# Performance work log

Hardware: AMD Instinct MI355X
Metric: run time of the kernel (lower is better)

The kernel has to match this reference:

```python
import jax, jax.numpy as jnp
import numpy as np

COMMITMENT = 1.0

def setup_inputs() -> dict:
    key = jax.random.key(0)
    k1, k2 = jax.random.split(key)
    x = jax.random.normal(k1, (32, 64, 64, 64), dtype=jnp.float32)       # [B, D, H, W]
    emb_w = jax.random.normal(k2, (512, 64), dtype=jnp.float32)          # [K, D] codebook
    return {"x": x, "emb_w": emb_w}

def reference(x, emb_w):
    B, D, H, W = x.shape
    K = emb_w.shape[0]
    # permute channels last and flatten: [B*H*W, D]
    xp = jnp.transpose(x, (0, 2, 3, 1))
    flat = xp.reshape(-1, D)
    # squared-distance matrix [N, K] via ||a||^2 + ||b||^2 - 2 a.b
    distances = (jnp.sum(flat * flat, axis=1, keepdims=True)
                 + jnp.sum(emb_w * emb_w, axis=1)
                 - 2.0 * jnp.matmul(flat, emb_w.T))
    encoding_flat = jnp.argmin(distances, axis=1)                        # [N]
    quantized = emb_w[encoding_flat].reshape(B, H, W, D)                 # gather
    quantized = jnp.transpose(quantized, (0, 3, 1, 2))                   # back to [B, D, H, W]
    # commitment loss: mse(stop_grad(quantized), x)
    e_latent_loss = jnp.mean((jax.lax.stop_gradient(quantized) - x) ** 2)
    loss = COMMITMENT * e_latent_loss
    # straight-through estimator
    quantized_st = x + jax.lax.stop_gradient(quantized - x)
    encoding = encoding_flat.reshape(B, H, W)
    return quantized_st, encoding, distances, loss
```

## Files before the change

kernel.cpp:

```cpp
#include <hip/hip_runtime.h>

typedef short short8 __attribute__((ext_vector_type(8)));
typedef float f32x4 __attribute__((ext_vector_type(4)));

#define EPS 0.012f

__device__ __forceinline__ unsigned short rne_bf16(float v) {
    unsigned u = __float_as_uint(v);
    unsigned r = u + 0x7FFFu + ((u >> 16) & 1u);
    return (unsigned short)(r >> 16);
}
__device__ __forceinline__ float bf16_to_f(unsigned short h) {
    return __uint_as_float(((unsigned)h) << 16);
}
__device__ __forceinline__ int xsw(int row, int d4) {
    return row * 64 + (d4 ^ ((row & 15) << 2));
}

#define MFMA(a,b,c) __builtin_amdgcn_mfma_f32_16x16x32_bf16((a),(b),(c),0,0,0)

__global__ __launch_bounds__(512, 4) void vq_kernel(
    const float* __restrict__ x, const float* __restrict__ emb,
    float* __restrict__ out_q, float* __restrict__ out_enc,
    float* __restrict__ out_dist, float* __restrict__ out_loss)
{
    __shared__ __align__(16) float xs[128 * 64];
    __shared__ __align__(16) unsigned short ehi[128 * 64];
    __shared__ __align__(16) unsigned short elo[128 * 64];
    __shared__ float xpart[4][128];
    __shared__ float xx_s[128];
    __shared__ float ee_s[128];
    __shared__ int   enc_s[128];
    __shared__ float red_s[8];

    const int t   = threadIdx.x;
    const int bid = blockIdx.x;
    const int n_base = bid * 128;
    const int b   = bid >> 5;
    const int h0  = (bid & 31) * 2;
    const size_t xb0 = (size_t)b * 262144 + (size_t)h0 * 64;
    const int l  = t & 63;
    const int wv = t >> 6;

    {
        const int w  = t & 63;
        const int q  = t >> 6;
        const int hh = q & 1;
        const int c0 = q >> 1;
        const int row = hh * 64 + w;
        const size_t gb = xb0 + hh * 64 + w;
        float part = 0.f;
        #pragma unroll
        for (int cc = 0; cc < 4; ++cc) {
            int d4 = (c0 + cc * 4) * 4;
            float4 v;
            v.x = x[gb + (size_t)(d4 + 0) * 4096];
            v.y = x[gb + (size_t)(d4 + 1) * 4096];
            v.z = x[gb + (size_t)(d4 + 2) * 4096];
            v.w = x[gb + (size_t)(d4 + 3) * 4096];
            part = fmaf(v.x, v.x, part); part = fmaf(v.y, v.y, part);
            part = fmaf(v.z, v.z, part); part = fmaf(v.w, v.w, part);
            *(float4*)&xs[xsw(row, d4)] = v;
        }
        xpart[c0][row] = part;
    }
    __syncthreads();
    if (t < 128) xx_s[t] = (xpart[0][t] + xpart[1][t]) + (xpart[2][t] + xpart[3][t]);

    const int arow = wv * 16 + (l & 15);
    const int ad0  = (l >> 4) * 8;
    short8 ahi0, ahi1, alo0, alo1;
    {
        float va[16];
        *(float4*)&va[0]  = *(const float4*)&xs[xsw(arow, ad0)];
        *(float4*)&va[4]  = *(const float4*)&xs[xsw(arow, ad0 + 4)];
        *(float4*)&va[8]  = *(const float4*)&xs[xsw(arow, ad0 + 32)];
        *(float4*)&va[12] = *(const float4*)&xs[xsw(arow, ad0 + 36)];
        #pragma unroll
        for (int i = 0; i < 8; ++i) {
            unsigned short hb = rne_bf16(va[i]);
            ahi0[i] = (short)hb; alo0[i] = (short)rne_bf16(va[i] - bf16_to_f(hb));
            unsigned short hb2 = rne_bf16(va[8 + i]);
            ahi1[i] = (short)hb2; alo1[i] = (short)rne_bf16(va[8 + i] - bf16_to_f(hb2));
        }
    }
    __syncthreads();

    const int rlw0 = (l >> 4) * 4;
    const int n0   = n_base + wv * 16 + rlw0;
    float xx4[4];
    #pragma unroll
    for (int r = 0; r < 4; ++r) xx4[r] = xx_s[wv * 16 + rlw0 + r];

    float m1[4], m2[4]; int k1[4];
    #pragma unroll
    for (int r = 0; r < 4; ++r) { m1[r] = 3.4e38f; m2[r] = 3.4e38f; k1[r] = 0; }

    float* dbase = out_dist + (size_t)n0 * 512 + (l & 15);

    for (int kc = 0; kc < 4; ++kc) {
        __syncthreads();
        float s01[2];
        #pragma unroll
        for (int it = 0; it < 2; ++it) {
            int flat = t + it * 512;
            int kr = flat >> 3;
            int d0 = (flat & 7) * 8;
            const float* src = emb + (size_t)(kc * 128 + kr) * 64 + d0;
            float4 v0 = *(const float4*)src;
            float4 v1 = *(const float4*)(src + 4);
            float vv[8] = {v0.x, v0.y, v0.z, v0.w, v1.x, v1.y, v1.z, v1.w};
            short8 h8, l8; float s = 0.f;
            #pragma unroll
            for (int i = 0; i < 8; ++i) {
                s = fmaf(vv[i], vv[i], s);
                unsigned short hb = rne_bf16(vv[i]);
                h8[i] = (short)hb; l8[i] = (short)rne_bf16(vv[i] - bf16_to_f(hb));
            }
            int idx = kr * 64 + (d0 ^ ((kr & 7) << 3));
            *(short8*)&ehi[idx] = h8;
            *(short8*)&elo[idx] = l8;
            s01[it] = s;
        }
        #pragma unroll
        for (int m = 1; m < 8; m <<= 1) {
            s01[0] += __shfl_xor(s01[0], m, 64);
            s01[1] += __shfl_xor(s01[1], m, 64);
        }
        if ((t & 7) == 0) {
            ee_s[t >> 3]        = s01[0];
            ee_s[64 + (t >> 3)] = s01[1];
        }
        __syncthreads();

        #pragma unroll 1
        for (int kt = 0; kt < 8; ++kt) {
            int kl  = kt * 16 + (l & 15);
            int bix = kl * 64;
            int bsw = (kl & 7) << 3;
            int bd0 = (l >> 4) * 8;
            short8 bh0 = *(short8*)&ehi[bix + (bd0 ^ bsw)];
            short8 bh1 = *(short8*)&ehi[bix + ((bd0 + 32) ^ bsw)];
            short8 bl0 = *(short8*)&elo[bix + (bd0 ^ bsw)];
            short8 bl1 = *(short8*)&elo[bix + ((bd0 + 32) ^ bsw)];
            f32x4 accA = {0.f, 0.f, 0.f, 0.f};
            f32x4 accB = {0.f, 0.f, 0.f, 0.f};
            accA = MFMA(ahi0, bh0, accA);
            accB = MFMA(ahi1, bh1, accB);
            accA = MFMA(alo0, bh0, accA);
            accB = MFMA(alo1, bh1, accB);
            accA = MFMA(ahi0, bl0, accA);
            accB = MFMA(ahi1, bl1, accB);
            float eek = ee_s[kl];
            int kg = kc * 128 + kl;
            float* dp = dbase + kc * 128 + kt * 16;
            #pragma unroll
            for (int r = 0; r < 4; ++r) {
                float dist = fmaf(accA[r] + accB[r], -2.f, xx4[r] + eek);
                dp[(size_t)r * 512] = dist;
                if (dist < m1[r]) { m2[r] = m1[r]; m1[r] = dist; k1[r] = kg; }
                else if (dist < m2[r]) m2[r] = dist;
            }
        }
    }

    __syncthreads();

    float lacc = 0.f;
    {
        const unsigned long long gmask = 0xFFFFull << ((l >> 4) << 4);
        #pragma unroll 1
        for (int r = 0; r < 4; ++r) {
            float bv = m1[r]; int bk = k1[r];
            #pragma unroll
            for (int m = 1; m < 16; m <<= 1) {
                float ov = __shfl_xor(bv, m, 64);
                int   ok = __shfl_xor(bk, m, 64);
                if (ov < bv || (ov == bv && ok < bk)) { bv = ov; bk = ok; }
            }
            float thr = bv + EPS;
            unsigned long long b1 = __ballot(m1[r] <= thr);
            unsigned long long b2 = __ballot(m2[r] <= thr);
            int enc = bk; float lossv = bv;
            if (__popcll(b1 & gmask) > 1 || (b2 & gmask) != 0ULL) {
                const int rowg = wv * 16 + rlw0 + r;
                const float* drow = out_dist + (size_t)(n_base + rowg) * 512 + (l & 15) * 32;
                double bestv = 1e300; int bestk = 0x7fffffff;
                #pragma unroll 1
                for (int c4 = 0; c4 < 8; ++c4) {
                    float4 dv = *(const float4*)(drow + c4 * 4);
                    float dvv[4] = {dv.x, dv.y, dv.z, dv.w};
                    #pragma unroll 1
                    for (int j = 0; j < 4; ++j) {
                        if (dvv[j] <= thr) {
                            int k = (l & 15) * 32 + c4 * 4 + j;
                            const float* er = emb + k * 64;
                            double s = 0.0;
                            #pragma unroll 4
                            for (int d = 0; d < 64; d += 4) {
                                float4 ev = *(const float4*)(er + d);
                                float4 xv = *(const float4*)&xs[xsw(rowg, d)];
                                double d0_ = (double)xv.x - (double)ev.x;
                                double d1_ = (double)xv.y - (double)ev.y;
                                double d2_ = (double)xv.z - (double)ev.z;
                                double d3_ = (double)xv.w - (double)ev.w;
                                s += d0_ * d0_ + d1_ * d1_ + d2_ * d2_ + d3_ * d3_;
                            }
                            if (s < bestv) { bestv = s; bestk = k; }
                        }
                    }
                }
                #pragma unroll
                for (int m = 1; m < 16; m <<= 1) {
                    double ov = __shfl_xor(bestv, m, 64);
                    int   ok  = __shfl_xor(bestk, m, 64);
                    if (ov < bestv || (ov == bestv && ok < bestk)) { bestv = ov; bestk = ok; }
                }
                enc = bestk;
                if ((l & 15) == 0 && enc != bk)
                    lossv = out_dist[(size_t)(n_base + rowg) * 512 + enc];
            }
            if ((l & 15) == 0) {
                enc_s[wv * 16 + rlw0 + r] = enc;
                out_enc[n0 + r] = (float)enc;
                lacc += lossv;
            }
        }
    }
    #pragma unroll
    for (int m = 32; m >= 1; m >>= 1) lacc += __shfl_down(lacc, m, 64);
    if (l == 0) red_s[wv] = lacc;
    __syncthreads();
    if (t == 0) {
        float tot = 0.f;
        #pragma unroll
        for (int i = 0; i < 8; ++i) tot += red_s[i];
        atomicAdd(out_loss, tot * (1.0f / 8388608.0f));
    }

    {
        const int w   = t & 63;
        const int q   = t >> 6;
        const int hh  = q & 1;
        const int dg  = q >> 1;
        const int row = hh * 64 + w;
        const int e   = enc_s[row];
        const float* er = emb + e * 64 + dg * 16;
        float* qp = out_q + xb0 + (size_t)(dg * 16) * 4096 + hh * 64 + w;
        #pragma unroll
        for (int qi = 0; qi < 4; ++qi) {
            float4 q4 = *(const float4*)(er + qi * 4);
            qp[(size_t)(qi * 4 + 0) * 4096] = q4.x;
            qp[(size_t)(qi * 4 + 1) * 4096] = q4.y;
            qp[(size_t)(qi * 4 + 2) * 4096] = q4.z;
            qp[(size_t)(qi * 4 + 3) * 4096] = q4.w;
        }
    }
}

extern "C" void kernel_launch(void* const* d_in, const int* in_sizes, int n_in,
                              void* d_out, int out_size, void* d_ws, size_t ws_size,
                              hipStream_t stream) {
    const float* x   = (const float*)d_in[0];
    const float* emb = (const float*)d_in[1];

    float* out_q    = (float*)d_out;
    float* out_enc  = out_q + 8388608;
    float* out_dist = out_enc + 131072;
    float* out_loss = out_dist + 67108864;

    hipMemsetAsync(out_loss, 0, sizeof(float), stream);
    vq_kernel<<<1024, 512, 0, stream>>>(x, emb, out_q, out_enc, out_dist, out_loss);
}
```

Measured before the change: 111.6 us.

## Precompute bf16 hi/lo codebook in prep kernel and stream B operands from global

Adds a small prep kernel that splits the codebook into bf16 hi/lo halves, pre-arranged in MFMA fragment order, and computes the row norms into workspace. The main kernel no longer converts the codebook per block into LDS. It reads B fragments straight from global/L2 with no per-chunk barriers. Blocks shrink to 64 rows and 256 threads with a 2048-block grid, cutting LDS use and raising occupancy. The cost is an extra kernel launch, and every block now fetches the codebook from global memory instead of shared memory.

```diff
diff --git a/kernel.cpp b/kernel.cpp
--- a/kernel.cpp
+++ b/kernel.cpp
@@ -19,36 +19,57 @@
 
 #define MFMA(a,b,c) __builtin_amdgcn_mfma_f32_16x16x32_bf16((a),(b),(c),0,0,0)
 
-__global__ __launch_bounds__(512, 4) void vq_kernel(
+__global__ __launch_bounds__(64) void prep_kernel(
+    const float* __restrict__ emb, unsigned short* __restrict__ whi,
+    unsigned short* __restrict__ wlo, float* __restrict__ wee)
+{
+    const int k = blockIdx.x * 64 + threadIdx.x;
+    const float* src = emb + k * 64;
+    float nrm = 0.f;
+    #pragma unroll
+    for (int g = 0; g < 8; ++g) {
+        float4 v0 = *(const float4*)(src + g * 8);
+        float4 v1 = *(const float4*)(src + g * 8 + 4);
+        float vv[8] = {v0.x, v0.y, v0.z, v0.w, v1.x, v1.y, v1.z, v1.w};
+        short8 h8, l8;
+        #pragma unroll
+        for (int i = 0; i < 8; ++i) {
+            nrm = fmaf(vv[i], vv[i], nrm);
+            unsigned short hb = rne_bf16(vv[i]);
+            h8[i] = (short)hb;
+            l8[i] = (short)rne_bf16(vv[i] - bf16_to_f(hb));
+        }
+        *(short8*)(whi + k * 64 + g * 8) = h8;
+        *(short8*)(wlo + k * 64 + g * 8) = l8;
+    }
+    wee[k] = nrm;
+}
+
+__global__ __launch_bounds__(256, 5) void vq_kernel(
     const float* __restrict__ x, const float* __restrict__ emb,
+    const unsigned short* __restrict__ whi, const unsigned short* __restrict__ wlo,
+    const float* __restrict__ wee,
     float* __restrict__ out_q, float* __restrict__ out_enc,
     float* __restrict__ out_dist, float* __restrict__ out_loss)
 {
-    __shared__ __align__(16) float xs[128 * 64];
-    __shared__ __align__(16) unsigned short ehi[128 * 64];
-    __shared__ __align__(16) unsigned short elo[128 * 64];
-    __shared__ float xpart[4][128];
-    __shared__ float xx_s[128];
-    __shared__ float ee_s[128];
-    __shared__ int   enc_s[128];
-    __shared__ float red_s[8];
+    __shared__ __align__(16) float xs[64 * 64];
+    __shared__ float ee_s[512];
+    __shared__ float xpart[4][64];
+    __shared__ float xx_s[64];
+    __shared__ int   enc_s[64];
+    __shared__ float red_s[4];
 
     const int t   = threadIdx.x;
     const int bid = blockIdx.x;
-    const int n_base = bid * 128;
-    const int b   = bid >> 5;
-    const int h0  = (bid & 31) * 2;
-    const size_t xb0 = (size_t)b * 262144 + (size_t)h0 * 64;
+    const int n_base = bid * 64;
+    const size_t xbase = (size_t)(bid >> 6) * 262144 + (size_t)(bid & 63) * 64;
     const int l  = t & 63;
     const int wv = t >> 6;
 
     {
         const int w  = t & 63;
-        const int q  = t >> 6;
-        const int hh = q & 1;
-        const int c0 = q >> 1;
-        const int row = hh * 64 + w;
-        const size_t gb = xb0 + hh * 64 + w;
+        const int c0 = t >> 6;
+        const size_t gb = xbase + w;
         float part = 0.f;
         #pragma unroll
         for (int cc = 0; cc < 4; ++cc) {
@@ -60,12 +81,14 @@
             v.w = x[gb + (size_t)(d4 + 3) * 4096];
             part = fmaf(v.x, v.x, part); part = fmaf(v.y, v.y, part);
             part = fmaf(v.z, v.z, part); part = fmaf(v.w, v.w, part);
-            *(float4*)&xs[xsw(row, d4)] = v;
-        }
-        xpart[c0][row] = part;
-    }
-    __syncthreads();
-    if (t < 128) xx_s[t] = (xpart[0][t] + xpart[1][t]) + (xpart[2][t] + xpart[3][t]);
+            *(float4*)&xs[xsw(w, d4)] = v;
+        }
+        xpart[c0][w] = part;
+        ee_s[t]       = wee[t];
+        ee_s[t + 256] = wee[t + 256];
+    }
+    __syncthreads();
+    if (t < 64) xx_s[t] = (xpart[0][t] + xpart[1][t]) + (xpart[2][t] + xpart[3][t]);
 
     const int arow = wv * 16 + (l & 15);
     const int ad0  = (l >> 4) * 8;
@@ -97,70 +120,34 @@
     for (int r = 0; r < 4; ++r) { m1[r] = 3.4e38f; m2[r] = 3.4e38f; k1[r] = 0; }
 
     float* dbase = out_dist + (size_t)n0 * 512 + (l & 15);
-
-    for (int kc = 0; kc < 4; ++kc) {
-        __syncthreads();
-        float s01[2];
-        #pragma unroll
-        for (int it = 0; it < 2; ++it) {
-            int flat = t + it * 512;
-            int kr = flat >> 3;
-            int d0 = (flat & 7) * 8;
-            const float* src = emb + (size_t)(kc * 128 + kr) * 64 + d0;
-            float4 v0 = *(const float4*)src;
-            float4 v1 = *(const float4*)(src + 4);
-            float vv[8] = {v0.x, v0.y, v0.z, v0.w, v1.x, v1.y, v1.z, v1.w};
-            short8 h8, l8; float s = 0.f;
-            #pragma unroll
-            for (int i = 0; i < 8; ++i) {
-                s = fmaf(vv[i], vv[i], s);
-                unsigned short hb = rne_bf16(vv[i]);
-                h8[i] = (short)hb; l8[i] = (short)rne_bf16(vv[i] - bf16_to_f(hb));
-            }
-            int idx = kr * 64 + (d0 ^ ((kr & 7) << 3));
-            *(short8*)&ehi[idx] = h8;
-            *(short8*)&elo[idx] = l8;
-            s01[it] = s;
-        }
-        #pragma unroll
-        for (int m = 1; m < 8; m <<= 1) {
-            s01[0] += __shfl_xor(s01[0], m, 64);
-            s01[1] += __shfl_xor(s01[1], m, 64);
-        }
-        if ((t & 7) == 0) {
-            ee_s[t >> 3]        = s01[0];
-            ee_s[64 + (t >> 3)] = s01[1];
-        }
-        __syncthreads();
-
-        #pragma unroll 1
-        for (int kt = 0; kt < 8; ++kt) {
-            int kl  = kt * 16 + (l & 15);
-            int bix = kl * 64;
-            int bsw = (kl & 7) << 3;
-            int bd0 = (l >> 4) * 8;
-            short8 bh0 = *(short8*)&ehi[bix + (bd0 ^ bsw)];
-            short8 bh1 = *(short8*)&ehi[bix + ((bd0 + 32) ^ bsw)];
-            short8 bl0 = *(short8*)&elo[bix + (bd0 ^ bsw)];
-            short8 bl1 = *(short8*)&elo[bix + ((bd0 + 32) ^ bsw)];
-            f32x4 accA = {0.f, 0.f, 0.f, 0.f};
-            f32x4 accB = {0.f, 0.f, 0.f, 0.f};
-            accA = MFMA(ahi0, bh0, accA);
-            accB = MFMA(ahi1, bh1, accB);
-            accA = MFMA(alo0, bh0, accA);
-            accB = MFMA(alo1, bh1, accB);
-            accA = MFMA(ahi0, bl0, accA);
-            accB = MFMA(ahi1, bl1, accB);
-            float eek = ee_s[kl];
-            int kg = kc * 128 + kl;
-            float* dp = dbase + kc * 128 + kt * 16;
-            #pragma unroll
-            for (int r = 0; r < 4; ++r) {
-                float dist = fmaf(accA[r] + accB[r], -2.f, xx4[r] + eek);
-                dp[(size_t)r * 512] = dist;
-                if (dist < m1[r]) { m2[r] = m1[r]; m1[r] = dist; k1[r] = kg; }
-                else if (dist < m2[r]) m2[r] = dist;
-            }
+    const short8* Hbase = (const short8*)whi;
+    const short8* Lbase = (const short8*)wlo;
+    const int bidx = (l & 15) * 8 + (l >> 4);
+
+    #pragma unroll 4
+    for (int kt = 0; kt < 32; ++kt) {
+        const int o = kt * 128 + bidx;
+        short8 bh0 = Hbase[o];
+        short8 bh1 = Hbase[o + 4];
+        short8 bl0 = Lbase[o];
+        short8 bl1 = Lbase[o + 4];
+        f32x4 accA = {0.f, 0.f, 0.f, 0.f};
+        f32x4 accB = {0.f, 0.f, 0.f, 0.f};
+        accA = MFMA(ahi0, bh0, accA);
+        accB = MFMA(ahi1, bh1, accB);
+        accA = MFMA(alo0, bh0, accA);
+        accB = MFMA(alo1, bh1, accB);
+        accA = MFMA(ahi0, bl0, accA);
+        accB = MFMA(ahi1, bl1, accB);
+        const int kl = kt * 16 + (l & 15);
+        float eek = ee_s[kl];
+        float* dp = dbase + kt * 16;
+        #pragma unroll
+        for (int r = 0; r < 4; ++r) {
+            float dist = fmaf(accA[r] + accB[r], -2.f, xx4[r] + eek);
+            dp[(size_t)r * 512] = dist;
+            if (dist < m1[r]) { m2[r] = m1[r]; m1[r] = dist; k1[r] = kl; }
+            else if (dist < m2[r]) m2[r] = dist;
         }
     }
 
@@ -231,22 +218,15 @@
     for (int m = 32; m >= 1; m >>= 1) lacc += __shfl_down(lacc, m, 64);
     if (l == 0) red_s[wv] = lacc;
     __syncthreads();
-    if (t == 0) {
-        float tot = 0.f;
-        #pragma unroll
-        for (int i = 0; i < 8; ++i) tot += red_s[i];
-        atomicAdd(out_loss, tot * (1.0f / 8388608.0f));
-    }
-
-    {
-        const int w   = t & 63;
-        const int q   = t >> 6;
-        const int hh  = q & 1;
-        const int dg  = q >> 1;
-        const int row = hh * 64 + w;
-        const int e   = enc_s[row];
+    if (t == 0)
+        atomicAdd(out_loss, (red_s[0] + red_s[1] + red_s[2] + red_s[3]) * (1.0f / 8388608.0f));
+
+    {
+        const int w  = t & 63;
+        const int dg = t >> 6;
+        const int e  = enc_s[w];
         const float* er = emb + e * 64 + dg * 16;
-        float* qp = out_q + xb0 + (size_t)(dg * 16) * 4096 + hh * 64 + w;
+        float* qp = out_q + xbase + (size_t)(dg * 16) * 4096 + w;
         #pragma unroll
         for (int qi = 0; qi < 4; ++qi) {
             float4 q4 = *(const float4*)(er + qi * 4);
@@ -269,6 +249,12 @@
     float* out_dist = out_enc + 131072;
     float* out_loss = out_dist + 67108864;
 
+    unsigned short* whi = (unsigned short*)d_ws;
+    unsigned short* wlo = whi + 32768;
+    float*          wee = (float*)(whi + 65536);
+
     hipMemsetAsync(out_loss, 0, sizeof(float), stream);
-    vq_kernel<<<1024, 512, 0, stream>>>(x, emb, out_q, out_enc, out_dist, out_loss);
-}
+    prep_kernel<<<8, 64, 0, stream>>>(emb, whi, wlo, wee);
+    vq_kernel<<<2048, 256, 0, stream>>>(x, emb, whi, wlo, wee,
+                                        out_q, out_enc, out_dist, out_loss);
+}
```

Measured after the change: 185.0 us. 1.66x slower.
